# Performance work log

Measured on AMD Instinct MI355X. Metric: run time of the kernel, lower is better.

Reference implementation:

```python
import jax, jax.numpy as jnp
import numpy as np

DIM = 64; Hh = 128; Ww = 128; Bz = 4
N = 8      # d_state
R = 4      # dt_rank = ceil(dim/16)
K = 4      # depthwise conv kernel
NB = 4     # number of CrossMambaBlocks (spa, spe, spa_cross, spe_cross)


def setup_inputs() -> dict:
    key = jax.random.key(0)
    ks = jax.random.split(key, 16)
    f32 = jnp.float32
    D = DIM
    rn = lambda k, shp, s: jax.random.normal(k, shp, f32) * s
    inp = {
        "img1": rn(ks[0], (Bz, D, Hh, Ww), 1.0),
        "img2": rn(ks[1], (Bz, D, Hh, Ww), 1.0),
        "img1_sum": rn(ks[2], (Bz, D, Hh, Ww), 1.0),
        "img2_sum": rn(ks[3], (Bz, D, Hh, Ww), 1.0),
        # LayerNorm params for norm0/norm1 of each block
        "ln_g0": jnp.ones((NB, D), f32), "ln_b0": jnp.zeros((NB, D), f32),
        "ln_g1": jnp.ones((NB, D), f32), "ln_b1": jnp.zeros((NB, D), f32),
        # Mamba projections (in_proj -> x,z from input0; in_proj_e -> extra embedding path)
        "W_in": rn(ks[4], (NB, D, 2 * D), D ** -0.5),
        "W_ine": rn(ks[5], (NB, D, D), D ** -0.5),
        # per-direction depthwise causal conv
        "convW": rn(ks[6], (NB, 2, D, K), K ** -0.5),
        "convB": jnp.zeros((NB, 2, D), f32),
        # x_proj (dt, B, C) computed from the cross-modal embedding (v7 cross variant)
        "W_x": rn(ks[7], (NB, 2, D, R + 2 * N), D ** -0.5),
        "W_dt": rn(ks[8], (NB, 2, R, D), R ** -0.5),
        "b_dt": jnp.full((NB, 2, D), -4.6, f32),  # softplus ~ 0.01
        "A_log": jnp.log(jnp.broadcast_to(jnp.arange(1, N + 1, dtype=f32), (NB, 2, D, N))),
        "Dp": jnp.ones((NB, 2, D), f32),
        "W_out": rn(ks[9], (NB, D, D), D ** -0.5),
        "b_out": jnp.zeros((NB, D), f32),
        # FusionMamba.out_proj
        "W_fo": rn(ks[10], (D, D), D ** -0.5),
        "b_fo": jnp.zeros((D,), f32),
    }
    return inp


def _ln(x, g, b):
    m = x.mean(-1, keepdims=True)
    v = ((x - m) ** 2).mean(-1, keepdims=True)
    return (x - m) * jax.lax.rsqrt(v + 1e-5) * g + b


def _causal_conv(x, w, b):
    # x: [B, L, D], w: [D, K] depthwise causal conv
    xt = x.transpose(0, 2, 1)  # [B, D, L]
    out = jax.lax.conv_general_dilated(xt, w[:, None, :], (1,), [(K - 1, 0)],
                                       feature_group_count=w.shape[0])
    return out.transpose(0, 2, 1) + b


def _selective_scan(x, dt, Bm, Cm, A):
    # x, dt: [B, L, D]; Bm, Cm: [B, L, N]; A: [D, N]
    def step(h, t):
        x_t, dt_t, B_t, C_t = t  # [B,D],[B,D],[B,N],[B,N]
        dA = jnp.exp(dt_t[:, :, None] * A)                       # [B,D,N]
        h = h * dA + (dt_t * x_t)[:, :, None] * B_t[:, None, :]  # [B,D,N]
        y = jnp.einsum('bdn,bn->bd', h, C_t)
        return h, y
    h0 = jnp.zeros((x.shape[0], x.shape[2], A.shape[1]), x.dtype)
    xs = (x.transpose(1, 0, 2), dt.transpose(1, 0, 2),
          Bm.transpose(1, 0, 2), Cm.transpose(1, 0, 2))
    _, ys = jax.lax.scan(step, h0, xs)
    return ys.transpose(1, 0, 2)  # [B, L, D]


def _cross_mamba_block(x0, x1, i, p):
    # x0, x1: [B, L, D]; bidirectional cross Mamba (bimamba v7, sum of directions)
    skip = x0
    a = _ln(x0, p['ln_g0'][i], p['ln_b0'][i])
    e = _ln(x1, p['ln_g1'][i], p['ln_b1'][i])
    xz = a @ p['W_in'][i]
    x, z = jnp.split(xz, 2, axis=-1)
    ee = e @ p['W_ine'][i]  # cross-modal embedding drives dt/B/C
    y = 0.0
    for d in range(2):
        xd = x if d == 0 else x[:, ::-1]
        ed = ee if d == 0 else ee[:, ::-1]
        zd = z if d == 0 else z[:, ::-1]
        xc = jax.nn.silu(_causal_conv(xd, p['convW'][i, d], p['convB'][i, d]))
        dbl = ed @ p['W_x'][i, d]
        dtr, Bm, Cm = dbl[..., :R], dbl[..., R:R + N], dbl[..., R + N:]
        dt = jax.nn.softplus(dtr @ p['W_dt'][i, d] + p['b_dt'][i, d])
        A = -jnp.exp(p['A_log'][i, d])
        yd = _selective_scan(xc, dt, Bm, Cm, A) + xc * p['Dp'][i, d]
        yd = yd * jax.nn.silu(zd)
        if d == 1:
            yd = yd[:, ::-1]
        y = y + yd
    return y @ p['W_out'][i] + p['b_out'][i] + skip


def reference(img1, img2, img1_sum, img2_sum, ln_g0, ln_b0, ln_g1, ln_b1,
              W_in, W_ine, convW, convB, W_x, W_dt, b_dt, A_log, Dp,
              W_out, b_out, W_fo, b_fo):
    p = dict(ln_g0=ln_g0, ln_b0=ln_b0, ln_g1=ln_g1, ln_b1=ln_b1, W_in=W_in,
             W_ine=W_ine, convW=convW, convB=convB, W_x=W_x, W_dt=W_dt,
             b_dt=b_dt, A_log=A_log, Dp=Dp, W_out=W_out, b_out=b_out)
    b, c, h, w = img1.shape
    flat = lambda t: t.reshape(b, c, h * w).transpose(0, 2, 1)   # b c h w -> b (hw) c
    unflat = lambda t: t.transpose(0, 2, 1).reshape(b, c, h, w)
    x1, x2, s1, s2 = flat(img1), flat(img2), flat(img1_sum), flat(img2_sum)
    x1 = _cross_mamba_block(x1, s1, 0, p)  # spa layer
    x2 = _cross_mamba_block(x2, s2, 1, p)  # spe layer
    spa = _cross_mamba_block(x1, x2, 2, p)
    spe = _cross_mamba_block(x2, x1, 3, p)
    fusion = (spa + spe) @ W_fo + b_fo
    out = unflat(fusion)
    return (unflat(x1) + out, unflat(x2) + out, img1_sum, img2_sum)
```

## Files before the change

### kernel.cpp

```cpp
#include <hip/hip_runtime.h>
#include <hip/hip_bf16.h>

#define BZ 4
#define DD 64
#define LL 16384
#define NN 8
#define BLD ((size_t)BZ*DD*LL)
#define BML ((size_t)BZ*20*LL)

__device__ __forceinline__ float silu_(float x){ return __fdividef(x, 1.f + __expf(-x)); }
__device__ __forceinline__ float softplus_(float x){ return (x > 20.f) ? x : __logf(1.f + __expf(x)); }


__global__ __launch_bounds__(256)
void k_in2(const float* __restrict__ s0a, const float* __restrict__ s1a,
           const float* __restrict__ s0b, const float* __restrict__ s1b,
           const float* __restrict__ lng0, const float* __restrict__ lnb0,
           const float* __restrict__ lng1, const float* __restrict__ lnb1,
           const float* __restrict__ W_in, const float* __restrict__ W_ine,
           const float* __restrict__ W_x, int i0,
           float* __restrict__ XBa, float* __restrict__ ZBa,
           float* __restrict__ XBb, float* __restrict__ ZBb,
           float* __restrict__ M00, float* __restrict__ M01,
           float* __restrict__ M10, float* __restrict__ M11)
{
  const int sel  = blockIdx.x >> 8;
  const int pi   = sel & 1;
  const int path = sel >> 1;
  const int pos = (blockIdx.x & 255)*256 + threadIdx.x;
  const int b = pos >> 14;
  const int l = pos & (LL-1);
  const int i = i0 + pi;

  if (path == 0){
    const float* src0 = pi ? s0b : s0a;
    float a[DD];
    #pragma unroll
    for (int ch=0; ch<DD; ++ch) a[ch] = src0[((size_t)(b*DD+ch))*LL + l];
    float m=0.f;
    #pragma unroll
    for (int k=0;k<DD;++k) m += a[k];
    m *= (1.f/DD);
    float v=0.f;
    #pragma unroll
    for (int k=0;k<DD;++k){ float d=a[k]-m; v += d*d; }
    v *= (1.f/DD);
    const float rs = rsqrtf(v + 1e-5f);
    #pragma unroll
    for (int k=0;k<DD;++k) a[k] = (a[k]-m)*rs*lng0[i*DD+k] + lnb0[i*DD+k];

    const float* Wi = W_in + (size_t)i*DD*2*DD;
    float* xrow = (pi ? XBb : XBa) + ((size_t)b*LL + l)*DD;
    float* zrow = (pi ? ZBb : ZBa) + ((size_t)b*LL + l)*DD;
    for (int g=0; g<8; ++g){
      float acc[16];
      #pragma unroll
      for (int j=0;j<16;++j) acc[j]=0.f;
      #pragma unroll
      for (int k=0;k<DD;++k){
        const float av = a[k];
        const float* wr = Wi + k*128 + g*16;
        #pragma unroll
        for (int j=0;j<16;++j) acc[j] = fmaf(av, wr[j], acc[j]);
      }
      float* drow = (g<4) ? (xrow + g*16) : (zrow + (g-4)*16);
      #pragma unroll
      for (int q=0;q<4;++q)
        ((float4*)drow)[q] = make_float4(acc[4*q],acc[4*q+1],acc[4*q+2],acc[4*q+3]);
    }
  } else {
    const float* src1 = pi ? s1b : s1a;
    float e[DD];
    #pragma unroll
    for (int ch=0; ch<DD; ++ch) e[ch] = src1[((size_t)(b*DD+ch))*LL + l];
    float m=0.f;
    #pragma unroll
    for (int k=0;k<DD;++k) m += e[k];
    m *= (1.f/DD);
    float v=0.f;
    #pragma unroll
    for (int k=0;k<DD;++k){ float d=e[k]-m; v += d*d; }
    v *= (1.f/DD);
    const float rs = rsqrtf(v + 1e-5f);
    #pragma unroll
    for (int k=0;k<DD;++k) e[k] = (e[k]-m)*rs*lng1[i*DD+k] + lnb1[i*DD+k];

    const float* We  = W_ine + (size_t)i*DD*DD;
    const float* Wx0 = W_x + ((size_t)(i*2+0)*DD)*20;
    const float* Wx1 = W_x + ((size_t)(i*2+1)*DD)*20;
    float acc0[20], acc1[20];
    #pragma unroll
    for (int j=0;j<20;++j){ acc0[j]=0.f; acc1[j]=0.f; }
    for (int gg=0; gg<4; ++gg){
      float eeg[16];
      #pragma unroll
      for (int j=0;j<16;++j) eeg[j]=0.f;
      #pragma unroll
      for (int k=0;k<DD;++k){
        const float ev = e[k];
        const float* wr = We + k*DD + gg*16;
        #pragma unroll
        for (int j=0;j<16;++j) eeg[j] = fmaf(ev, wr[j], eeg[j]);
      }
      const float* w0 = Wx0 + (size_t)(gg*16)*20;
      const float* w1 = Wx1 + (size_t)(gg*16)*20;
      #pragma unroll
      for (int jj=0;jj<16;++jj){
        const float s = eeg[jj];
        #pragma unroll
        for (int j=0;j<20;++j){
          acc0[j] = fmaf(s, w0[jj*20+j], acc0[j]);
          acc1[j] = fmaf(s, w1[jj*20+j], acc1[j]);
        }
      }
    }
    float* mrow0 = (pi ? M10 : M00) + ((size_t)b*LL + l)*20;
    float* mrow1 = (pi ? M11 : M01) + ((size_t)b*LL + l)*20;
    #pragma unroll
    for (int q=0;q<5;++q){
      ((float4*)mrow0)[q] = make_float4(acc0[4*q],acc0[4*q+1],acc0[4*q+2],acc0[4*q+3]);
      ((float4*)mrow1)[q] = make_float4(acc1[4*q],acc1[4*q+1],acc1[4*q+2],acc1[4*q+3]);
    }
  }
}

template<int NC2, bool PASSC>
__global__ __launch_bounds__(64)
void k_scan4(const float* __restrict__ XBa, const float* __restrict__ XBb,
             const float* __restrict__ ZBa, const float* __restrict__ ZBb,
             float* __restrict__ Y0, float* __restrict__ Y1,
             float* __restrict__ Y2, float* __restrict__ Y3,
             const float* __restrict__ M00, const float* __restrict__ M01,
             const float* __restrict__ M10, const float* __restrict__ M11,
             const float* __restrict__ convW, const float* __restrict__ convB,
             const float* __restrict__ Wdt, const float* __restrict__ bdt,
             const float* __restrict__ Alog, const float* __restrict__ Dpw, int i0,
             float* __restrict__ PP, float* __restrict__ FF,
             const float* __restrict__ HH)
{
  const int TC2 = LL / NC2;
  const size_t SC2 = (size_t)BZ*NC2*DD*NN;
  const int inst = blockIdx.x / (BZ*NC2);
  const int rb = blockIdx.x - inst*(BZ*NC2);
  const int c = rb & (NC2-1);
  const int b = rb / NC2;
  const int ch = threadIdx.x;
  const int pi = inst >> 1, d = inst & 1;
  const int id = (i0+pi)*2 + d;

  const float* xb = pi ? XBb : XBa;
  const float* zb = pi ? ZBb : ZBa;
  const float* meta = (inst==0)?M00:(inst==1)?M01:(inst==2)?M10:M11;
  float* yb = (inst==0)?Y0:(inst==1)?Y1:(inst==2)?Y2:Y3;

  float cw[4];
  #pragma unroll
  for (int k=0;k<4;++k) cw[k] = convW[((size_t)id*DD+ch)*4 + k];
  const float cb = convB[id*DD + ch];
  float wd[4];
  #pragma unroll
  for (int r=0;r<4;++r) wd[r] = Wdt[((size_t)id*4 + r)*DD + ch];
  const float bd = bdt[id*DD + ch];
  float An[NN];
  #pragma unroll
  for (int n=0;n<NN;++n) An[n] = -__expf(Alog[((size_t)id*DD+ch)*NN + n]);
  const float dp = PASSC ? Dpw[id*DD + ch] : 0.f;

  bool fastA = true;
  #pragma unroll
  for (int n=0;n<NN;++n) fastA = fastA && (fabsf(An[n] + (float)(n+1)) < 1e-3f);

  const size_t sbase = (size_t)inst*SC2 + ((size_t)(b*NC2+c)*DD + ch)*NN;
  float h[NN], P[NN];
  float Sdt = 0.f;
  if (PASSC){
    #pragma unroll
    for (int n=0;n<NN;++n) h[n] = HH[sbase+n];
  } else {
    #pragma unroll
    for (int n=0;n<NN;++n){ h[n]=0.f; P[n]=1.f; }
  }

  const int stp = d ? -1 : 1;
  const int t0  = d ? (LL-1 - c*TC2) : (c*TC2);

  float p1=0.f, p2=0.f, p3=0.f;
  {
    int tp = t0 - stp;
    if ((unsigned)tp < LL) p1 = xb[((size_t)b*LL+tp)*DD+ch];
    tp -= stp;
    if ((unsigned)tp < LL) p2 = xb[((size_t)b*LL+tp)*DD+ch];
    tp -= stp;
    if ((unsigned)tp < LL) p3 = xb[((size_t)b*LL+tp)*DD+ch];
  }

  int t = t0;
  for (int s=0; s<TC2; ++s, t+=stp){
    const size_t row = (size_t)b*LL + t;
    const float xv = xb[row*DD+ch];
    const float xc = silu_(cb + cw[0]*p3 + cw[1]*p2 + cw[2]*p1 + cw[3]*xv);
    p3=p2; p2=p1; p1=xv;

    const float* mt = meta + row*20;
    const float dpre = bd + mt[0]*wd[0] + mt[1]*wd[1] + mt[2]*wd[2] + mt[3]*wd[3];
    const float dt = softplus_(dpre);
    const float u = dt*xc;

    float dA[NN];
    if (fastA){
      const float E = __expf(-dt);
      const float E2 = E*E, E4 = E2*E2;
      dA[0]=E;    dA[1]=E2;    dA[2]=E2*E;  dA[3]=E4;
      dA[4]=E4*E; dA[5]=E4*E2; dA[6]=E4*E2*E; dA[7]=E4*E4;
      Sdt += dt;
    } else {
      #pragma unroll
      for (int n=0;n<NN;++n) dA[n] = __expf(dt*An[n]);
    }

    if (!PASSC){
      #pragma unroll
      for (int n=0;n<NN;++n){
        h[n] = fmaf(h[n], dA[n], u*mt[4+n]);
      }
      if (!fastA){
        #pragma unroll
        for (int n=0;n<NN;++n) P[n] *= dA[n];
      }
    } else {
      float y = 0.f;
      #pragma unroll
      for (int n=0;n<NN;++n){
        h[n] = fmaf(h[n], dA[n], u*mt[4+n]);
        y = fmaf(h[n], mt[12+n], y);
      }
      const float zv = zb[row*DD+ch];
      yb[row*DD + ch] = (y + xc*dp)*silu_(zv);
    }
  }

  if (!PASSC){
    if (fastA){
      const float E = __expf(-Sdt);
      const float E2 = E*E, E4 = E2*E2;
      P[0]=E;    P[1]=E2;    P[2]=E2*E;  P[3]=E4;
      P[4]=E4*E; P[5]=E4*E2; P[6]=E4*E2*E; P[7]=E4*E4;
    }
    #pragma unroll
    for (int n=0;n<NN;++n){ PP[sbase+n] = P[n]; FF[sbase+n] = h[n]; }
  }
}

template<int NC2>
__global__ __launch_bounds__(256)
void k_mid4(const float* __restrict__ PP, const float* __restrict__ FF,
            float* __restrict__ HH)
{
  const size_t SC2 = (size_t)BZ*NC2*DD*NN;
  const int inst = blockIdx.x >> 3;
  const int idx = (blockIdx.x & 7)*256 + threadIdx.x;
  const int b  = idx >> 9;
  const int cn = idx & 511;
  const size_t base = (size_t)inst*SC2;
  float h = 0.f;
  #pragma unroll 4
  for (int c=0; c<NC2; ++c){
    const size_t a2 = base + (((size_t)(b*NC2+c))<<9) + cn;
    HH[a2] = h;
    h = h*PP[a2] + FF[a2];
  }
}

__global__ __launch_bounds__(256)
void k_out2(const float* __restrict__ Y0, const float* __restrict__ Y1,
            const float* __restrict__ Y2, const float* __restrict__ Y3,
            const float* __restrict__ skipA, const float* __restrict__ skipB,
            const float* __restrict__ Wout, const float* __restrict__ bout,
            float* __restrict__ dstA, float* __restrict__ dstB)
{
  const int pi = blockIdx.x >> 8;
  const int pos = (blockIdx.x & 255)*256 + threadIdx.x;
  const int b = pos >> 14;
  const int l = pos & (LL-1);
  const size_t row = ((size_t)b*LL + l)*DD;

  const float* Ya = pi ? Y2 : Y0;
  const float* Yb = pi ? Y3 : Y1;
  const float* skip = pi ? skipB : skipA;
  float* dst = pi ? dstB : dstA;
  const float* Wo = Wout + (size_t)pi*DD*DD;
  const float* bo = bout + pi*DD;

  float y[DD];
  {
    const float4* pa = (const float4*)(Ya + row);
    const float4* pb = (const float4*)(Yb + row);
    #pragma unroll
    for (int q=0;q<16;++q){
      float4 v0=pa[q], v1=pb[q];
      y[4*q]=v0.x+v1.x; y[4*q+1]=v0.y+v1.y; y[4*q+2]=v0.z+v1.z; y[4*q+3]=v0.w+v1.w;
    }
  }
  for (int g=0; g<4; ++g){
    float acc[16];
    #pragma unroll
    for (int j=0;j<16;++j) acc[j]=0.f;
    #pragma unroll
    for (int k=0;k<DD;++k){
      const float av = y[k];
      const float* wr = Wo + k*DD + g*16;
      #pragma unroll
      for (int j=0;j<16;++j) acc[j] = fmaf(av, wr[j], acc[j]);
    }
    #pragma unroll
    for (int j=0;j<16;++j){
      const int col = g*16 + j;
      const size_t o = ((size_t)(b*DD+col))*LL + l;
      dst[o] = acc[j] + bo[col] + skip[o];
    }
  }
}

__global__ __launch_bounds__(256)
void k_tail(const float* __restrict__ Y0, const float* __restrict__ Y1,
            const float* __restrict__ Y2, const float* __restrict__ Y3,
            const float* __restrict__ X1, const float* __restrict__ X2,
            const float* __restrict__ Wout, const float* __restrict__ bout,
            const float* __restrict__ Wfo, const float* __restrict__ bfo,
            float* __restrict__ ob)
{
  const int gid = blockIdx.x*256 + threadIdx.x;
  const int b = gid >> 14;
  const int l = gid & (LL-1);
  const size_t row = ((size_t)b*LL + l)*DD;

  float s[DD];
  float y[DD];
  {
    const float4* p0 = (const float4*)(Y0 + row);
    const float4* p1 = (const float4*)(Y1 + row);
    #pragma unroll
    for (int q=0;q<16;++q){
      float4 v0=p0[q], v1=p1[q];
      y[4*q]=v0.x+v1.x; y[4*q+1]=v0.y+v1.y; y[4*q+2]=v0.z+v1.z; y[4*q+3]=v0.w+v1.w;
    }
    const float* Wo = Wout + 2*DD*DD;
    const float* bo = bout + 2*DD;
    for (int g=0; g<4; ++g){
      float acc[16];
      #pragma unroll
      for (int j=0;j<16;++j) acc[j]=0.f;
      #pragma unroll
      for (int k=0;k<DD;++k){
        const float av = y[k];
        const float* wr = Wo + k*DD + g*16;
        #pragma unroll
        for (int j=0;j<16;++j) acc[j] = fmaf(av, wr[j], acc[j]);
      }
      #pragma unroll
      for (int j=0;j<16;++j){
        const int col = g*16 + j;
        s[col] = acc[j] + bo[col] + X1[((size_t)(b*DD+col))*LL + l];
      }
    }
  }
  {
    const float4* p0 = (const float4*)(Y2 + row);
    const float4* p1 = (const float4*)(Y3 + row);
    #pragma unroll
    for (int q=0;q<16;++q){
      float4 v0=p0[q], v1=p1[q];
      y[4*q]=v0.x+v1.x; y[4*q+1]=v0.y+v1.y; y[4*q+2]=v0.z+v1.z; y[4*q+3]=v0.w+v1.w;
    }
    const float* Wo = Wout + 3*DD*DD;
    const float* bo = bout + 3*DD;
    for (int g=0; g<4; ++g){
      float acc[16];
      #pragma unroll
      for (int j=0;j<16;++j) acc[j]=0.f;
      #pragma unroll
      for (int k=0;k<DD;++k){
        const float av = y[k];
        const float* wr = Wo + k*DD + g*16;
        #pragma unroll
        for (int j=0;j<16;++j) acc[j] = fmaf(av, wr[j], acc[j]);
      }
      #pragma unroll
      for (int j=0;j<16;++j){
        const int col = g*16 + j;
        s[col] += acc[j] + bo[col] + X2[((size_t)(b*DD+col))*LL + l];
      }
    }
  }
  for (int g=0; g<4; ++g){
    float acc[16];
    #pragma unroll
    for (int j=0;j<16;++j) acc[j]=0.f;
    #pragma unroll
    for (int k=0;k<DD;++k){
      const float av = s[k];
      const float* wr = Wfo + k*DD + g*16;
      #pragma unroll
      for (int j=0;j<16;++j) acc[j] = fmaf(av, wr[j], acc[j]);
    }
    #pragma unroll
    for (int j=0;j<16;++j){
      const int col = g*16 + j;
      const size_t o = ((size_t)(b*DD+col))*LL + l;
      const float fu = acc[j] + bfo[col];
      ob[o]       = X1[o] + fu;
      ob[BLD + o] = X2[o] + fu;
    }
  }
}

__global__ __launch_bounds__(256)
void k_copy4(const float* __restrict__ s, float* __restrict__ o)
{
  const size_t i = (size_t)blockIdx.x*256 + threadIdx.x;
  ((float4*)o)[i] = ((const float4*)s)[i];
}

__global__ __launch_bounds__(256)
void f_in(const float* __restrict__ src0, const float* __restrict__ src1,
          const float* __restrict__ lng0, const float* __restrict__ lnb0,
          const float* __restrict__ lng1, const float* __restrict__ lnb1,
          const float* __restrict__ W_in, const float* __restrict__ W_ine,
          const float* __restrict__ W_x, int i,
          float* __restrict__ XB, float* __restrict__ ZB,
          float* __restrict__ M0, float* __restrict__ M1)
{
  const int gid = blockIdx.x*256 + threadIdx.x;
  const int b = gid >> 14;
  const int l = gid & (LL-1);

  float a[DD];
  for (int ch=0; ch<DD; ++ch) a[ch] = src0[((size_t)(b*DD+ch))*LL + l];
  {
    float m=0.f; for (int k=0;k<DD;++k) m += a[k];  m *= (1.f/DD);
    float v=0.f; for (int k=0;k<DD;++k){ float d=a[k]-m; v += d*d; }  v *= (1.f/DD);
    float rs = rsqrtf(v + 1e-5f);
    for (int k=0;k<DD;++k) a[k] = (a[k]-m)*rs*lng0[i*DD+k] + lnb0[i*DD+k];
  }
  const float* Wi = W_in + (size_t)i*DD*2*DD;
  float* xrow = XB + ((size_t)b*LL + l)*DD;
  float* zrow = ZB + ((size_t)b*LL + l)*DD;
  for (int g=0; g<8; ++g){
    float acc[16];
    #pragma unroll
    for (int j=0;j<16;++j) acc[j]=0.f;
    for (int k=0;k<DD;++k){
      const float av = a[k];
      const float* wr = Wi + k*128 + g*16;
      #pragma unroll
      for (int j=0;j<16;++j) acc[j] = fmaf(av, wr[j], acc[j]);
    }
    float* drow = (g<4) ? (xrow + g*16) : (zrow + (g-4)*16);
    #pragma unroll
    for (int q=0;q<4;++q)
      ((float4*)drow)[q] = make_float4(acc[4*q],acc[4*q+1],acc[4*q+2],acc[4*q+3]);
  }
  float e[DD], ee[DD];
  for (int ch=0; ch<DD; ++ch) e[ch] = src1[((size_t)(b*DD+ch))*LL + l];
  {
    float m=0.f; for (int k=0;k<DD;++k) m += e[k];  m *= (1.f/DD);
    float v=0.f; for (int k=0;k<DD;++k){ float d=e[k]-m; v += d*d; }  v *= (1.f/DD);
    float rs = rsqrtf(v + 1e-5f);
    for (int k=0;k<DD;++k) e[k] = (e[k]-m)*rs*lng1[i*DD+k] + lnb1[i*DD+k];
  }
  const float* We = W_ine + (size_t)i*DD*DD;
  for (int m2=0; m2<DD; ++m2){
    float s = 0.f;
    for (int k=0;k<DD;++k) s = fmaf(e[k], We[k*DD + m2], s);
    ee[m2] = s;
  }
  for (int d=0; d<2; ++d){
    float acc[20];
    #pragma unroll
    for (int j=0;j<20;++j) acc[j]=0.f;
    for (int m2=0; m2<DD; ++m2){
      const float ev = ee[m2];
      const float* wr = W_x + ((size_t)(i*2+d)*DD + m2)*20;
      #pragma unroll
      for (int j=0;j<20;++j) acc[j] = fmaf(ev, wr[j], acc[j]);
    }
    float* mrow = (d ? M1 : M0) + ((size_t)b*LL + l)*20;
    #pragma unroll
    for (int q=0;q<5;++q)
      ((float4*)mrow)[q] = make_float4(acc[4*q],acc[4*q+1],acc[4*q+2],acc[4*q+3]);
  }
}

template<int DIR, bool PASSC>
__global__ __launch_bounds__(64)
void f_scan(const float* __restrict__ xb, const float* __restrict__ zb,
            float* __restrict__ yb, const float* __restrict__ meta,
            const float* __restrict__ convW, const float* __restrict__ convB,
            const float* __restrict__ Wdt, const float* __restrict__ bdt,
            const float* __restrict__ Alog, const float* __restrict__ Dpw, int id,
            float* __restrict__ Pb, float* __restrict__ Fb,
            const float* __restrict__ Hin)
{
  const int ch = threadIdx.x;
  const int c  = blockIdx.x & 255;
  const int b  = blockIdx.x >> 8;

  float cw[4];
  for (int k=0;k<4;++k) cw[k] = convW[((size_t)id*DD+ch)*4 + k];
  const float cb = convB[id*DD + ch];
  float wd[4]; for (int r=0;r<4;++r) wd[r] = Wdt[((size_t)id*4 + r)*DD + ch];
  const float bd = bdt[id*DD + ch];
  float An[NN]; for (int n=0;n<NN;++n) An[n] = -__expf(Alog[((size_t)id*DD+ch)*NN + n]);
  const float dp = PASSC ? Dpw[id*DD + ch] : 0.f;

  const size_t sbase = ((size_t)(b*256+c)*DD + ch)*NN;
  float h[NN], P[NN];
  if (PASSC){
    #pragma unroll
    for (int n=0;n<NN;++n) h[n] = Hin[sbase+n];
  } else {
    #pragma unroll
    for (int n=0;n<NN;++n){ h[n]=0.f; P[n]=1.f; }
  }

  int t0, stp;
  if (DIR==0){ t0 = c*64;        stp =  1; }
  else       { t0 = LL-1 - c*64; stp = -1; }

  float p1=0.f, p2=0.f, p3=0.f;
  {
    int tp = t0 - stp;
    if ((unsigned)tp < LL) p1 = xb[((size_t)b*LL+tp)*DD+ch];
    tp -= stp;
    if ((unsigned)tp < LL) p2 = xb[((size_t)b*LL+tp)*DD+ch];
    tp -= stp;
    if ((unsigned)tp < LL) p3 = xb[((size_t)b*LL+tp)*DD+ch];
  }

  int t = t0;
  for (int s=0; s<64; ++s, t+=stp){
    const size_t row = (size_t)b*LL + t;
    const float xv = xb[row*DD+ch];
    const float xc = silu_(cb + cw[0]*p3 + cw[1]*p2 + cw[2]*p1 + cw[3]*xv);
    p3=p2; p2=p1; p1=xv;

    const float* mt = meta + row*20;
    const float dpre = bd + mt[0]*wd[0] + mt[1]*wd[1] + mt[2]*wd[2] + mt[3]*wd[3];
    const float dt = softplus_(dpre);
    const float u = dt*xc;

    if (!PASSC){
      #pragma unroll
      for (int n=0;n<NN;++n){
        const float dA = __expf(dt*An[n]);
        h[n] = h[n]*dA + u*mt[4+n];
        P[n] *= dA;
      }
    } else {
      float y = 0.f;
      #pragma unroll
      for (int n=0;n<NN;++n){
        const float dA = __expf(dt*An[n]);
        h[n] = h[n]*dA + u*mt[4+n];
        y = fmaf(h[n], mt[12+n], y);
      }
      const float zv = zb[row*DD+ch];
      const float o = (y + xc*dp)*silu_(zv);
      float* yp = yb + row*DD + ch;
      if (DIR==0) *yp = o; else *yp += o;
    }
  }

  if (!PASSC){
    #pragma unroll
    for (int n=0;n<NN;++n){ Pb[sbase+n] = P[n]; Fb[sbase+n] = h[n]; }
  }
}

__global__ __launch_bounds__(256)
void f_mid(const float* __restrict__ Pb, const float* __restrict__ Fb,
           float* __restrict__ Hin)
{
  const int idx = blockIdx.x*256 + threadIdx.x;
  const int b  = idx >> 9;
  const int cn = idx & 511;
  float h = 0.f;
  #pragma unroll 4
  for (int c=0; c<256; ++c){
    const size_t a2 = (((size_t)(b*256+c))<<9) + cn;
    Hin[a2] = h;
    h = h*Pb[a2] + Fb[a2];
  }
}

template<int MODE>
__global__ __launch_bounds__(256)
void f_out(const float* __restrict__ YB, const float* __restrict__ skip,
           const float* __restrict__ Wo, const float* __restrict__ bo,
           float* __restrict__ dst)
{
  const int gid = blockIdx.x*256 + threadIdx.x;
  const int b = gid >> 14;
  const int l = gid & (LL-1);
  float y[DD];
  {
    const float4* s4 = (const float4*)(YB + ((size_t)b*LL + l)*DD);
    #pragma unroll
    for (int q=0;q<16;++q){ float4 v=s4[q]; y[4*q]=v.x; y[4*q+1]=v.y; y[4*q+2]=v.z; y[4*q+3]=v.w; }
  }
  for (int g=0; g<4; ++g){
    float acc[16];
    #pragma unroll
    for (int j=0;j<16;++j) acc[j]=0.f;
    for (int k=0;k<DD;++k){
      const float av = y[k];
      const float* wr = Wo + k*DD + g*16;
      #pragma unroll
      for (int j=0;j<16;++j) acc[j] = fmaf(av, wr[j], acc[j]);
    }
    #pragma unroll
    for (int j=0;j<16;++j){
      const int col = g*16 + j;
      const size_t o = ((size_t)(b*DD+col))*LL + l;
      float s = acc[j] + bo[col] + skip[o];
      if (MODE==1) s += dst[o];
      dst[o] = s;
    }
  }
}

__global__ __launch_bounds__(256)
void f_fuse(const float* __restrict__ FS, const float* __restrict__ X1,
            const float* __restrict__ X2, const float* __restrict__ Wfo,
            const float* __restrict__ bfo, float* __restrict__ ob)
{
  const int gid = blockIdx.x*256 + threadIdx.x;
  const int b = gid >> 14;
  const int l = gid & (LL-1);
  float fs[DD];
  for (int ch=0; ch<DD; ++ch) fs[ch] = FS[((size_t)(b*DD+ch))*LL + l];
  for (int g=0; g<4; ++g){
    float acc[16];
    #pragma unroll
    for (int j=0;j<16;++j) acc[j]=0.f;
    for (int k=0;k<DD;++k){
      const float av = fs[k];
      const float* wr = Wfo + k*DD + g*16;
      #pragma unroll
      for (int j=0;j<16;++j) acc[j] = fmaf(av, wr[j], acc[j]);
    }
    #pragma unroll
    for (int j=0;j<16;++j){
      const int col = g*16 + j;
      const size_t o = ((size_t)(b*DD+col))*LL + l;
      const float fu = acc[j] + bfo[col];
      ob[o]       = X1[o] + fu;
      ob[BLD + o] = X2[o] + fu;
    }
  }
}

extern "C" void kernel_launch(void* const* d_in, const int* in_sizes, int n_in,
                              void* d_out, int out_size, void* d_ws, size_t ws_size,
                              hipStream_t stream)
{
  static const int dictsz[21]  = {4194304,4194304,4194304,4194304,256,256,256,256,
                                  32768,16384,2048,512,10240,2048,512,4096,512,
                                  16384,256,4096,64};
  int map[21];
  bool okd = (n_in >= 21);
  if (okd) for (int i=0;i<21;++i) if (in_sizes[i] != dictsz[i]) { okd = false; break; }
  if (okd){
    for (int i=0;i<21;++i) map[i] = i;
  } else {
    bool used[64];
    for (int j=0;j<64;++j) used[j]=false;
    for (int i=0;i<21;++i){
      map[i] = -1;
      for (int j=0;j<n_in && j<64;++j)
        if (!used[j] && in_sizes[j]==dictsz[i]){ map[i]=j; used[j]=true; break; }
      if (map[i] < 0) map[i] = (i < n_in ? i : 0);
    }
  }

  const float* img1 = (const float*)d_in[map[0]];
  const float* img2 = (const float*)d_in[map[1]];
  const float* s1   = (const float*)d_in[map[2]];
  const float* s2   = (const float*)d_in[map[3]];
  const float* lng0 = (const float*)d_in[map[4]];
  const float* lnb0 = (const float*)d_in[map[5]];
  const float* lng1 = (const float*)d_in[map[6]];
  const float* lnb1 = (const float*)d_in[map[7]];
  const float* Win  = (const float*)d_in[map[8]];
  const float* Wine = (const float*)d_in[map[9]];
  const float* convW= (const float*)d_in[map[10]];
  const float* convB= (const float*)d_in[map[11]];
  const float* Wx   = (const float*)d_in[map[12]];
  const float* Wdt  = (const float*)d_in[map[13]];
  const float* bdt  = (const float*)d_in[map[14]];
  const float* Alog = (const float*)d_in[map[15]];
  const float* Dp   = (const float*)d_in[map[16]];
  const float* Wout = (const float*)d_in[map[17]];
  const float* bout = (const float*)d_in[map[18]];
  const float* Wfo  = (const float*)d_in[map[19]];
  const float* bfo  = (const float*)d_in[map[20]];

  float* ob = (float*)d_out;
  float* ws = (float*)d_ws;

  k_copy4<<<4096,256,0,stream>>>(s1, ob + 2*BLD);
  k_copy4<<<4096,256,0,stream>>>(s2, ob + 3*BLD);

  const size_t SCN512 = (size_t)BZ*512*DD*NN;
  const size_t SCN256 = (size_t)BZ*256*DD*NN;
  const size_t need512 = (10*BLD + 4*BML + 12*SCN512 + 64)*sizeof(float);
  const size_t need256 = (10*BLD + 4*BML + 12*SCN256 + 64)*sizeof(float);

  if (ws_size >= need256){
    const bool big = (ws_size >= need512);
    const size_t SC = big ? SCN512 : SCN256;
    float* X1  = ws;
    float* X2  = ws + 1*BLD;
    float* XBa = ws + 2*BLD;
    float* ZBa = ws + 3*BLD;
    float* XBb = ws + 4*BLD;
    float* ZBb = ws + 5*BLD;
    float* Y0  = ws + 6*BLD;
    float* Y1  = ws + 7*BLD;
    float* Y2  = ws + 8*BLD;
    float* Y3  = ws + 9*BLD;
    float* M00 = ws + 10*BLD;
    float* M01 = M00 + BML;
    float* M10 = M01 + BML;
    float* M11 = M10 + BML;
    float* PP  = M11 + BML;
    float* FF  = PP + 4*SC;
    float* HH  = FF + 4*SC;

    for (int pr=0; pr<2; ++pr){
      const int i0 = pr*2;
      if (pr==0)
        k_in2<<<1024,256,0,stream>>>(img1, s1, img2, s2, lng0,lnb0,lng1,lnb1,
                                     Win, Wine, Wx, 0, XBa,ZBa,XBb,ZBb, M00,M01,M10,M11);
      else
        k_in2<<<1024,256,0,stream>>>(X1, X2, X2, X1, lng0,lnb0,lng1,lnb1,
                                     Win, Wine, Wx, 2, XBa,ZBa,XBb,ZBb, M00,M01,M10,M11);
      if (big){
        k_scan4<512,false><<<4*BZ*512,64,0,stream>>>(XBa,XBb,ZBa,ZBb, Y0,Y1,Y2,Y3,
                                                     M00,M01,M10,M11, convW,convB,Wdt,bdt,Alog,Dp,
                                                     i0, PP,FF,HH);
        k_mid4<512><<<32,256,0,stream>>>(PP,FF,HH);
        k_scan4<512,true ><<<4*BZ*512,64,0,stream>>>(XBa,XBb,ZBa,ZBb, Y0,Y1,Y2,Y3,
                                                     M00,M01,M10,M11, convW,convB,Wdt,bdt,Alog,Dp,
                                                     i0, PP,FF,HH);
      } else {
        k_scan4<256,false><<<4*BZ*256,64,0,stream>>>(XBa,XBb,ZBa,ZBb, Y0,Y1,Y2,Y3,
                                                     M00,M01,M10,M11, convW,convB,Wdt,bdt,Alog,Dp,
                                                     i0, PP,FF,HH);
        k_mid4<256><<<32,256,0,stream>>>(PP,FF,HH);
        k_scan4<256,true ><<<4*BZ*256,64,0,stream>>>(XBa,XBb,ZBa,ZBb, Y0,Y1,Y2,Y3,
                                                     M00,M01,M10,M11, convW,convB,Wdt,bdt,Alog,Dp,
                                                     i0, PP,FF,HH);
      }
      if (pr==0)
        k_out2<<<512,256,0,stream>>>(Y0,Y1,Y2,Y3, img1,img2, Wout,bout, X1,X2);
      else
        k_tail<<<256,256,0,stream>>>(Y0,Y1,Y2,Y3, X1,X2, Wout,bout, Wfo,bfo, ob);
    }
    return;
  }

  float* X1 = ws;
  float* X2 = ws + 1*BLD;
  float* FS = ws + 2*BLD;
  float* XB = ws + 3*BLD;
  float* ZB = ws + 4*BLD;
  float* YB = ws + 5*BLD;
  float* M0 = ws + 6*BLD;
  float* M1 = M0 + BML;
  float* PP = M1 + BML;
  float* FF = PP + SCN256;
  float* HH = FF + SCN256;

  const size_t need = (6*BLD + 2*BML + 3*SCN256 + 64)*sizeof(float);
  if (ws_size < need) return;

  const float* bx0[4] = {img1, img2, X1, X2};
  const float* bx1[4] = {s1,   s2,   X2, X1};

  for (int i=0; i<4; ++i){
    f_in<<<256,256,0,stream>>>(bx0[i], bx1[i], lng0, lnb0, lng1, lnb1,
                               Win, Wine, Wx, i, XB, ZB, M0, M1);
    for (int d=0; d<2; ++d){
      const int id = i*2+d;
      const float* Md = d ? M1 : M0;
      if (d==0){
        f_scan<0,false><<<BZ*256,64,0,stream>>>(XB,nullptr,nullptr,Md,convW,convB,Wdt,bdt,Alog,nullptr,id,PP,FF,nullptr);
        f_mid<<<8,256,0,stream>>>(PP,FF,HH);
        f_scan<0,true ><<<BZ*256,64,0,stream>>>(XB,ZB,YB,Md,convW,convB,Wdt,bdt,Alog,Dp,id,nullptr,nullptr,HH);
      } else {
        f_scan<1,false><<<BZ*256,64,0,stream>>>(XB,nullptr,nullptr,Md,convW,convB,Wdt,bdt,Alog,nullptr,id,PP,FF,nullptr);
        f_mid<<<8,256,0,stream>>>(PP,FF,HH);
        f_scan<1,true ><<<BZ*256,64,0,stream>>>(XB,ZB,YB,Md,convW,convB,Wdt,bdt,Alog,Dp,id,nullptr,nullptr,HH);
      }
    }
    const float* Wop = Wout + (size_t)i*DD*DD;
    const float* bop = bout + (size_t)i*DD;
    if      (i==0) f_out<0><<<256,256,0,stream>>>(YB, img1, Wop, bop, X1);
    else if (i==1) f_out<0><<<256,256,0,stream>>>(YB, img2, Wop, bop, X2);
    else if (i==2) f_out<0><<<256,256,0,stream>>>(YB, X1,   Wop, bop, FS);
    else           f_out<1><<<256,256,0,stream>>>(YB, X2,   Wop, bop, FS);
  }
  f_fuse<<<256,256,0,stream>>>(FS, X1, X2, Wfo, bfo, ob);
}
```

Measured before the change: 811.4 us.

## Split projection kernels across output column groups to raise block-level parallelism

The input projection now gives the x and z outputs to separate blocks (three roles per instance instead of two). The output projections are split so each block computes one 16-column group, which multiplies the grid size. The fused tail is broken into a per-block output-projection kernel writing row-major intermediates and a separate fusion-projection kernel. The two summary copies are merged into one launch. The aim is more blocks and less per-thread serial work for these low-occupancy kernels, paid for by redundant LayerNorm and y reads per column group plus an extra intermediate round trip through memory.

```diff
diff --git a/kernel.cpp b/kernel.cpp
--- a/kernel.cpp
+++ b/kernel.cpp
@@ -25,14 +25,14 @@
            float* __restrict__ M10, float* __restrict__ M11)
 {
   const int sel  = blockIdx.x >> 8;
-  const int pi   = sel & 1;
-  const int path = sel >> 1;
+  const int pi   = sel / 3;
+  const int role = sel - 3*pi;
   const int pos = (blockIdx.x & 255)*256 + threadIdx.x;
   const int b = pos >> 14;
   const int l = pos & (LL-1);
   const int i = i0 + pi;
 
-  if (path == 0){
+  if (role < 2){
     const float* src0 = pi ? s0b : s0a;
     float a[DD];
     #pragma unroll
@@ -50,23 +50,22 @@
     for (int k=0;k<DD;++k) a[k] = (a[k]-m)*rs*lng0[i*DD+k] + lnb0[i*DD+k];
 
     const float* Wi = W_in + (size_t)i*DD*2*DD;
-    float* xrow = (pi ? XBb : XBa) + ((size_t)b*LL + l)*DD;
-    float* zrow = (pi ? ZBb : ZBa) + ((size_t)b*LL + l)*DD;
-    for (int g=0; g<8; ++g){
+    float* drow = ((role==0) ? (pi ? XBb : XBa) : (pi ? ZBb : ZBa)) + ((size_t)b*LL + l)*DD;
+    const int gbase = role*4;
+    for (int g=0; g<4; ++g){
       float acc[16];
       #pragma unroll
       for (int j=0;j<16;++j) acc[j]=0.f;
       #pragma unroll
       for (int k=0;k<DD;++k){
         const float av = a[k];
-        const float* wr = Wi + k*128 + g*16;
+        const float* wr = Wi + k*128 + (gbase+g)*16;
         #pragma unroll
         for (int j=0;j<16;++j) acc[j] = fmaf(av, wr[j], acc[j]);
       }
-      float* drow = (g<4) ? (xrow + g*16) : (zrow + (g-4)*16);
       #pragma unroll
       for (int q=0;q<4;++q)
-        ((float4*)drow)[q] = make_float4(acc[4*q],acc[4*q+1],acc[4*q+2],acc[4*q+3]);
+        ((float4*)(drow + g*16))[q] = make_float4(acc[4*q],acc[4*q+1],acc[4*q+2],acc[4*q+3]);
     }
   } else {
     const float* src1 = pi ? s1b : s1a;
@@ -220,9 +219,7 @@
 
     if (!PASSC){
       #pragma unroll
-      for (int n=0;n<NN;++n){
-        h[n] = fmaf(h[n], dA[n], u*mt[4+n]);
-      }
+      for (int n=0;n<NN;++n) h[n] = fmaf(h[n], dA[n], u*mt[4+n]);
       if (!fastA){
         #pragma unroll
         for (int n=0;n<NN;++n) P[n] *= dA[n];
@@ -278,7 +275,9 @@
             const float* __restrict__ Wout, const float* __restrict__ bout,
             float* __restrict__ dstA, float* __restrict__ dstB)
 {
-  const int pi = blockIdx.x >> 8;
+  const int sel = blockIdx.x >> 8;
+  const int pi = sel >> 2;
+  const int g  = sel & 3;
   const int pos = (blockIdx.x & 255)*256 + threadIdx.x;
   const int b = pos >> 14;
   const int l = pos & (LL-1);
@@ -301,117 +300,130 @@
       y[4*q]=v0.x+v1.x; y[4*q+1]=v0.y+v1.y; y[4*q+2]=v0.z+v1.z; y[4*q+3]=v0.w+v1.w;
     }
   }
-  for (int g=0; g<4; ++g){
-    float acc[16];
-    #pragma unroll
-    for (int j=0;j<16;++j) acc[j]=0.f;
-    #pragma unroll
-    for (int k=0;k<DD;++k){
-      const float av = y[k];
-      const float* wr = Wo + k*DD + g*16;
-      #pragma unroll
-      for (int j=0;j<16;++j) acc[j] = fmaf(av, wr[j], acc[j]);
-    }
-    #pragma unroll
-    for (int j=0;j<16;++j){
-      const int col = g*16 + j;
-      const size_t o = ((size_t)(b*DD+col))*LL + l;
-      dst[o] = acc[j] + bo[col] + skip[o];
-    }
-  }
-}
-
-__global__ __launch_bounds__(256)
-void k_tail(const float* __restrict__ Y0, const float* __restrict__ Y1,
-            const float* __restrict__ Y2, const float* __restrict__ Y3,
-            const float* __restrict__ X1, const float* __restrict__ X2,
-            const float* __restrict__ Wout, const float* __restrict__ bout,
-            const float* __restrict__ Wfo, const float* __restrict__ bfo,
-            float* __restrict__ ob)
-{
-  const int gid = blockIdx.x*256 + threadIdx.x;
-  const int b = gid >> 14;
-  const int l = gid & (LL-1);
+  float acc[16];
+  #pragma unroll
+  for (int j=0;j<16;++j) acc[j]=0.f;
+  #pragma unroll
+  for (int k=0;k<DD;++k){
+    const float av = y[k];
+    const float* wr = Wo + k*DD + g*16;
+    #pragma unroll
+    for (int j=0;j<16;++j) acc[j] = fmaf(av, wr[j], acc[j]);
+  }
+  #pragma unroll
+  for (int j=0;j<16;++j){
+    const int col = g*16 + j;
+    const size_t o = ((size_t)(b*DD+col))*LL + l;
+    dst[o] = acc[j] + bo[col] + skip[o];
+  }
+}
+
+__global__ __launch_bounds__(256)
+void k_o34(const float* __restrict__ Y0, const float* __restrict__ Y1,
+           const float* __restrict__ Y2, const float* __restrict__ Y3,
+           const float* __restrict__ X1, const float* __restrict__ X2,
+           const float* __restrict__ Wout, const float* __restrict__ bout,
+           float* __restrict__ FSa, float* __restrict__ FSb)
+{
+  const int sel = blockIdx.x >> 8;
+  const int wh = sel >> 2;
+  const int g  = sel & 3;
+  const int pos = (blockIdx.x & 255)*256 + threadIdx.x;
+  const int b = pos >> 14;
+  const int l = pos & (LL-1);
   const size_t row = ((size_t)b*LL + l)*DD;
 
-  float s[DD];
+  const float* Ya = wh ? Y2 : Y0;
+  const float* Yb = wh ? Y3 : Y1;
+  const float* skip = wh ? X2 : X1;
+  float* FS = wh ? FSb : FSa;
+  const float* Wo = Wout + (size_t)(2+wh)*DD*DD;
+  const float* bo = bout + (2+wh)*DD;
+
   float y[DD];
   {
-    const float4* p0 = (const float4*)(Y0 + row);
-    const float4* p1 = (const float4*)(Y1 + row);
+    const float4* pa = (const float4*)(Ya + row);
+    const float4* pb = (const float4*)(Yb + row);
     #pragma unroll
     for (int q=0;q<16;++q){
-      float4 v0=p0[q], v1=p1[q];
+      float4 v0=pa[q], v1=pb[q];
       y[4*q]=v0.x+v1.x; y[4*q+1]=v0.y+v1.y; y[4*q+2]=v0.z+v1.z; y[4*q+3]=v0.w+v1.w;
     }
-    const float* Wo = Wout + 2*DD*DD;
-    const float* bo = bout + 2*DD;
-    for (int g=0; g<4; ++g){
-      float acc[16];
-      #pragma unroll
-      for (int j=0;j<16;++j) acc[j]=0.f;
-      #pragma unroll
-      for (int k=0;k<DD;++k){
-        const float av = y[k];
-        const float* wr = Wo + k*DD + g*16;
-        #pragma unroll
-        for (int j=0;j<16;++j) acc[j] = fmaf(av, wr[j], acc[j]);
-      }
-      #pragma unroll
-      for (int j=0;j<16;++j){
-        const int col = g*16 + j;
-        s[col] = acc[j] + bo[col] + X1[((size_t)(b*DD+col))*LL + l];
-      }
-    }
-  }
+  }
+  float acc[16];
+  #pragma unroll
+  for (int j=0;j<16;++j) acc[j]=0.f;
+  #pragma unroll
+  for (int k=0;k<DD;++k){
+    const float av = y[k];
+    const float* wr = Wo + k*DD + g*16;
+    #pragma unroll
+    for (int j=0;j<16;++j) acc[j] = fmaf(av, wr[j], acc[j]);
+  }
+  float* frow = FS + row + g*16;
+  #pragma unroll
+  for (int q=0;q<4;++q){
+    const int j4 = 4*q;
+    make_float4(0,0,0,0);
+    float4 v;
+    v.x = acc[j4+0] + bo[g*16+j4+0] + skip[((size_t)(b*DD+g*16+j4+0))*LL + l];
+    v.y = acc[j4+1] + bo[g*16+j4+1] + skip[((size_t)(b*DD+g*16+j4+1))*LL + l];
+    v.z = acc[j4+2] + bo[g*16+j4+2] + skip[((size_t)(b*DD+g*16+j4+2))*LL + l];
+    v.w = acc[j4+3] + bo[g*16+j4+3] + skip[((size_t)(b*DD+g*16+j4+3))*LL + l];
+    ((float4*)frow)[q] = v;
+  }
+}
+
+__global__ __launch_bounds__(256)
+void k_fuse2(const float* __restrict__ FSa, const float* __restrict__ FSb,
+             const float* __restrict__ X1, const float* __restrict__ X2,
+             const float* __restrict__ Wfo, const float* __restrict__ bfo,
+             float* __restrict__ ob)
+{
+  const int g = blockIdx.x >> 8;
+  const int pos = (blockIdx.x & 255)*256 + threadIdx.x;
+  const int b = pos >> 14;
+  const int l = pos & (LL-1);
+  const size_t row = ((size_t)b*LL + l)*DD;
+
+  float fs[DD];
   {
-    const float4* p0 = (const float4*)(Y2 + row);
-    const float4* p1 = (const float4*)(Y3 + row);
+    const float4* pa = (const float4*)(FSa + row);
+    const float4* pb = (const float4*)(FSb + row);
     #pragma unroll
     for (int q=0;q<16;++q){
-      float4 v0=p0[q], v1=p1[q];
-      y[4*q]=v0.x+v1.x; y[4*q+1]=v0.y+v1.y; y[4*q+2]=v0.z+v1.z; y[4*q+3]=v0.w+v1.w;
-    }
-    const float* Wo = Wout + 3*DD*DD;
-    const float* bo = bout + 3*DD;
-    for (int g=0; g<4; ++g){
-      float acc[16];
-      #pragma unroll
-      for (int j=0;j<16;++j) acc[j]=0.f;
-      #pragma unroll
-      for (int k=0;k<DD;++k){
-        const float av = y[k];
-        const float* wr = Wo + k*DD + g*16;
-        #pragma unroll
-        for (int j=0;j<16;++j) acc[j] = fmaf(av, wr[j], acc[j]);
-      }
-      #pragma unroll
-      for (int j=0;j<16;++j){
-        const int col = g*16 + j;
-        s[col] += acc[j] + bo[col] + X2[((size_t)(b*DD+col))*LL + l];
-      }
-    }
-  }
-  for (int g=0; g<4; ++g){
-    float acc[16];
-    #pragma unroll
-    for (int j=0;j<16;++j) acc[j]=0.f;
-    #pragma unroll
-    for (int k=0;k<DD;++k){
-      const float av = s[k];
-      const float* wr = Wfo + k*DD + g*16;
-      #pragma unroll
-      for (int j=0;j<16;++j) acc[j] = fmaf(av, wr[j], acc[j]);
-    }
-    #pragma unroll
-    for (int j=0;j<16;++j){
-      const int col = g*16 + j;
-      const size_t o = ((size_t)(b*DD+col))*LL + l;
-      const float fu = acc[j] + bfo[col];
-      ob[o]       = X1[o] + fu;
-      ob[BLD + o] = X2[o] + fu;
-    }
-  }
+      float4 v0=pa[q], v1=pb[q];
+      fs[4*q]=v0.x+v1.x; fs[4*q+1]=v0.y+v1.y; fs[4*q+2]=v0.z+v1.z; fs[4*q+3]=v0.w+v1.w;
+    }
+  }
+  float acc[16];
+  #pragma unroll
+  for (int j=0;j<16;++j) acc[j]=0.f;
+  #pragma unroll
+  for (int k=0;k<DD;++k){
+    const float av = fs[k];
+    const float* wr = Wfo + k*DD + g*16;
+    #pragma unroll
+    for (int j=0;j<16;++j) acc[j] = fmaf(av, wr[j], acc[j]);
+  }
+  #pragma unroll
+  for (int j=0;j<16;++j){
+    const int col = g*16 + j;
+    const size_t o = ((size_t)(b*DD+col))*LL + l;
+    const float fu = acc[j] + bfo[col];
+    ob[o]       = X1[o] + fu;
+    ob[BLD + o] = X2[o] + fu;
+  }
+}
+
+__global__ __launch_bounds__(256)
+void k_copyboth(const float* __restrict__ s1, const float* __restrict__ s2,
+                float* __restrict__ o)
+{
+  const size_t gid = (size_t)blockIdx.x*256 + threadIdx.x;
+  const size_t half = BLD/4;
+  if (gid < half) ((float4*)(o        ))[gid]        = ((const float4*)s1)[gid];
+  else            ((float4*)(o + BLD ))[gid - half]  = ((const float4*)s2)[gid - half];
 }
 
 __global__ __launch_bounds__(256)
@@ -708,15 +720,14 @@
   float* ob = (float*)d_out;
   float* ws = (float*)d_ws;
 
-  k_copy4<<<4096,256,0,stream>>>(s1, ob + 2*BLD);
-  k_copy4<<<4096,256,0,stream>>>(s2, ob + 3*BLD);
-
   const size_t SCN512 = (size_t)BZ*512*DD*NN;
   const size_t SCN256 = (size_t)BZ*256*DD*NN;
   const size_t need512 = (10*BLD + 4*BML + 12*SCN512 + 64)*sizeof(float);
   const size_t need256 = (10*BLD + 4*BML + 12*SCN256 + 64)*sizeof(float);
 
   if (ws_size >= need256){
+    k_copyboth<<<8192,256,0,stream>>>(s1, s2, ob + 2*BLD);
+
     const bool big = (ws_size >= need512);
     const size_t SC = big ? SCN512 : SCN256;
     float* X1  = ws;
@@ -740,10 +751,10 @@
     for (int pr=0; pr<2; ++pr){
       const int i0 = pr*2;
       if (pr==0)
-        k_in2<<<1024,256,0,stream>>>(img1, s1, img2, s2, lng0,lnb0,lng1,lnb1,
+        k_in2<<<1536,256,0,stream>>>(img1, s1, img2, s2, lng0,lnb0,lng1,lnb1,
                                      Win, Wine, Wx, 0, XBa,ZBa,XBb,ZBb, M00,M01,M10,M11);
       else
-        k_in2<<<1024,256,0,stream>>>(X1, X2, X2, X1, lng0,lnb0,lng1,lnb1,
+        k_in2<<<1536,256,0,stream>>>(X1, X2, X2, X1, lng0,lnb0,lng1,lnb1,
                                      Win, Wine, Wx, 2, XBa,ZBa,XBb,ZBb, M00,M01,M10,M11);
       if (big){
         k_scan4<512,false><<<4*BZ*512,64,0,stream>>>(XBa,XBb,ZBa,ZBb, Y0,Y1,Y2,Y3,
@@ -762,13 +773,18 @@
                                                      M00,M01,M10,M11, convW,convB,Wdt,bdt,Alog,Dp,
                                                      i0, PP,FF,HH);
       }
-      if (pr==0)
-        k_out2<<<512,256,0,stream>>>(Y0,Y1,Y2,Y3, img1,img2, Wout,bout, X1,X2);
-      else
-        k_tail<<<256,256,0,stream>>>(Y0,Y1,Y2,Y3, X1,X2, Wout,bout, Wfo,bfo, ob);
+      if (pr==0){
+        k_out2<<<2048,256,0,stream>>>(Y0,Y1,Y2,Y3, img1,img2, Wout,bout, X1,X2);
+      } else {
+        k_o34<<<2048,256,0,stream>>>(Y0,Y1,Y2,Y3, X1,X2, Wout,bout, XBa, ZBa);
+        k_fuse2<<<1024,256,0,stream>>>(XBa, ZBa, X1, X2, Wfo, bfo, ob);
+      }
     }
     return;
   }
+
+  k_copy4<<<4096,256,0,stream>>>(s1, ob + 2*BLD);
+  k_copy4<<<4096,256,0,stream>>>(s2, ob + 3*BLD);
 
   float* X1 = ws;
   float* X2 = ws + 1*BLD;
```

After: 821.4 us. About the same (+1.2%).
